# Performance work log

Hardware: AMD Instinct MI355X
Metric: run time of the kernel (lower is better)

Reference implementation:

```python
import math
import jax, jax.numpy as jnp
import numpy as np

B, S, D, H = 2, 2048, 2048, 16
HD = D // H  # 128


def _rope_tables(seq_len, head_dim, theta=10000.0):
    freqs = 1.0 / (theta ** (np.arange(0, head_dim, 2, dtype=np.float32) / head_dim))
    t = np.arange(seq_len, dtype=np.float32)
    ang = np.outer(t, freqs)  # [S, HD/2]
    return jnp.asarray(np.cos(ang)), jnp.asarray(np.sin(ang))


def setup_inputs() -> dict:
    key = jax.random.key(0)
    ks = jax.random.split(key, 5)
    sc = 1.0 / math.sqrt(D)
    x = jax.random.normal(ks[0], (B, S, D), dtype=jnp.float32)
    wq = jax.random.normal(ks[1], (D, D), dtype=jnp.float32) * sc
    wk = jax.random.normal(ks[2], (D, D), dtype=jnp.float32) * sc
    wv = jax.random.normal(ks[3], (D, D), dtype=jnp.float32) * sc
    wo = jax.random.normal(ks[4], (D, D), dtype=jnp.float32) * sc
    freqs_cos, freqs_sin = _rope_tables(S, HD)
    # additive causal mask: 0 on/below diagonal, -inf above
    mask = jnp.where(jnp.tril(jnp.ones((S, S), dtype=bool)), 0.0, -jnp.inf).astype(jnp.float32)
    return {"x": x, "wq": wq, "wk": wk, "wv": wv, "wo": wo,
            "freqs_cos": freqs_cos, "freqs_sin": freqs_sin,
            "mask": mask, "start_pos": 0}


def _apply_rope(t, cos, sin):
    # t: [B, S, H, HD]; pairs (even, odd) rotated as complex numbers (LLaMA style)
    tr = t.reshape(*t.shape[:-1], HD // 2, 2)
    te, to = tr[..., 0], tr[..., 1]
    c = cos[None, :, None, :]
    s = sin[None, :, None, :]
    out_e = te * c - to * s
    out_o = te * s + to * c
    return jnp.stack([out_e, out_o], axis=-1).reshape(t.shape)


def reference(x, wq, wk, wv, wo, freqs_cos, freqs_sin, mask, start_pos):
    bsz, seqlen, _ = x.shape
    xq = (x @ wq.T).reshape(bsz, seqlen, H, HD)
    xk = (x @ wk.T).reshape(bsz, seqlen, H, HD)
    xv = (x @ wv.T).reshape(bsz, seqlen, H, HD)
    xq = _apply_rope(xq, freqs_cos, freqs_sin)
    xk = _apply_rope(xk, freqs_cos, freqs_sin)
    # n_rep == 1 so repeat_kv is identity
    scores = jnp.einsum('bqhd,bkhd->bhqk', xq, xk) / math.sqrt(HD)
    scores = scores + mask  # broadcast [S,S] over [B,H,S,S]
    probs = jax.nn.softmax(scores.astype(jnp.float32), axis=-1).astype(xq.dtype)
    out = jnp.einsum('bhqk,bkhd->bqhd', probs, xv).reshape(bsz, seqlen, -1)
    return out @ wo.T
```

## Files before the change

### kernel.cpp

```cpp
#include <hip/hip_runtime.h>


typedef __bf16 bf16_t;
typedef __bf16 bf16x4 __attribute__((ext_vector_type(4)));
typedef __bf16 bf16x8 __attribute__((ext_vector_type(8)));
typedef float  f32x4  __attribute__((ext_vector_type(4)));

#define DEV __device__ __forceinline__

DEV void async_copy16(const bf16_t* g, bf16_t* lds_uniform_base) {
    __builtin_amdgcn_global_load_lds(
        (const __attribute__((address_space(1))) void*)g,
        (__attribute__((address_space(3))) void*)lds_uniform_base,
        16, 0, 0);
}

__global__ void cast_all(const float* __restrict__ x,  const float* __restrict__ wq,
                         const float* __restrict__ wk, const float* __restrict__ wv,
                         const float* __restrict__ wo,
                         bf16_t* __restrict__ xb, bf16_t* __restrict__ W3,
                         bf16_t* __restrict__ wob)
{
    const int i = blockIdx.x * blockDim.x + threadIdx.x;
    const float4* src;
    bf16x4* dst;
    if (i < 2097152) {
        src = (const float4*)x + i;
        dst = (bf16x4*)xb + i;
    } else {
        const int j   = i - 2097152;
        const int r   = j >> 20;
        const int off = j & 1048575;
        const float* s4 = (r == 0) ? wq : (r == 1) ? wk : (r == 2) ? wv : wo;
        src = (const float4*)s4 + off;
        dst = (r < 3) ? ((bf16x4*)W3 + (long)r * 1048576 + off)
                      : ((bf16x4*)wob + off);
    }
    const float4 v = *src;
    bf16x4 o = { (bf16_t)v.x, (bf16_t)v.y, (bf16_t)v.z, (bf16_t)v.w };
    *dst = o;
}

__global__ __launch_bounds__(256)
void gemm_qkv(const bf16_t* __restrict__ A, const bf16_t* __restrict__ Bm,
              bf16_t* __restrict__ Qo, bf16_t* __restrict__ Ko,
              bf16_t* __restrict__ VTo,
              const float* __restrict__ cosT, const float* __restrict__ sinT)
{
    constexpr int K = 2048;
    __shared__ bf16_t As[128 * 64];
    __shared__ bf16_t Bs[128 * 64];

    const int tid  = threadIdx.x;
    const int w    = tid >> 6;
    const int lane = tid & 63;
    const int l16  = lane & 15;
    const int quad = lane >> 4;
    const int l7   = l16 & 7;
    const int wm   = w >> 1, wn = w & 1;

    const int id   = blockIdx.x;
    const int xcd  = id & 7;
    const int slot = id >> 3;
    const int nl   = slot % 6;
    const int ml   = slot / 6;
    const long n0  = (long)(xcd * 6 + nl) * 128;
    const long m0  = (long)ml * 128;

    f32x4 acc[4][4] = {};

    const bf16_t* Ag[4];
    const bf16_t* Bg[4];
    #pragma unroll
    for (int i = 0; i < 4; ++i) {
        const int c   = i * 256 + tid;
        const int row = c >> 3;
        const int col = ((c & 7) ^ (row & 7)) * 8;
        Ag[i] = A  + (m0 + row) * K + col;
        Bg[i] = Bm + (n0 + row) * K + col;
    }

    for (int k0 = 0; k0 < K; k0 += 64) {
        __syncthreads();
        #pragma unroll
        for (int i = 0; i < 4; ++i) {
            async_copy16(Ag[i] + k0, As + i * 2048 + w * 512);
            async_copy16(Bg[i] + k0, Bs + i * 2048 + w * 512);
        }
        __syncthreads();

        #pragma unroll
        for (int kc = 0; kc < 2; ++kc) {
            bf16x8 af[4], bfr[4];
            #pragma unroll
            for (int t = 0; t < 4; ++t) {
                const int cs = ((kc * 4 + quad) ^ l7) * 8;
                af[t]  = *(const bf16x8*)&As[(wm * 64 + t * 16 + l16) * 64 + cs];
                bfr[t] = *(const bf16x8*)&Bs[(wn * 64 + t * 16 + l16) * 64 + cs];
            }
            #pragma unroll
            for (int mt = 0; mt < 4; ++mt)
                #pragma unroll
                for (int nt = 0; nt < 4; ++nt)
                    acc[mt][nt] = __builtin_amdgcn_mfma_f32_16x16x32_bf16(
                        af[mt], bfr[nt], acc[mt][nt], 0, 0, 0);
        }
    }

    const int region = (int)(n0 >> 11);
    #pragma unroll
    for (int mt = 0; mt < 4; ++mt) {
        #pragma unroll
        for (int nt = 0; nt < 4; ++nt) {
            if (region < 2) {
                bf16_t* dst = (region == 0) ? Qo : Ko;
                #pragma unroll
                for (int r = 0; r < 4; ++r) {
                    const long m = m0 + wm * 64 + mt * 16 + quad * 4 + r;
                    const long n = n0 + wn * 64 + nt * 16 + l16;
                    float v = acc[mt][nt][r];
                    const float partner = __shfl_xor(v, 1);
                    const int d    = (int)n & 127;
                    const int fidx = ((int)m & 2047) * 64 + (d >> 1);
                    const float c = cosT[fidx], s = sinT[fidx];
                    v = ((int)n & 1) ? fmaf(partner, s, v * c)
                                     : (v * c - partner * s);
                    dst[m * 2048 + (n & 2047)] = (bf16_t)v;
                }
            } else {
                const long m  = m0 + wm * 64 + mt * 16 + quad * 4;
                const int  np = (int)(n0 + wn * 64 + nt * 16 + l16) - 4096;
                bf16x4 pk;
                #pragma unroll
                for (int r = 0; r < 4; ++r) pk[r] = (bf16_t)acc[mt][nt][r];
                const int b  = (int)(m >> 11);
                const int s0 = (int)m & 2047;
                const long idx = ((long)(b * 16 + (np >> 7)) * 128 + (np & 127)) * 2048 + s0;
                *(bf16x4*)&VTo[idx] = pk;
            }
        }
    }
}

__global__ __launch_bounds__(256)
void gemm_out(const bf16_t* __restrict__ A, const bf16_t* __restrict__ Bm,
              float* __restrict__ Cp)
{
    constexpr int K = 2048, N = 2048;
    __shared__ bf16_t As[128 * 64];
    __shared__ bf16_t Bs[128 * 64];

    const int tid  = threadIdx.x;
    const int w    = tid >> 6;
    const int lane = tid & 63;
    const int l16  = lane & 15;
    const int quad = lane >> 4;
    const int l7   = l16 & 7;
    const int wm   = w >> 1, wn = w & 1;

    const int id   = blockIdx.x;
    const int xcd  = id & 7;
    const int slot = id >> 3;
    const long n0  = (long)(xcd * 2 + (slot & 1)) * 128;
    const long m0  = (long)(slot >> 1) * 128;

    f32x4 acc[4][4] = {};

    const bf16_t* Ag[4];
    const bf16_t* Bg[4];
    #pragma unroll
    for (int i = 0; i < 4; ++i) {
        const int c   = i * 256 + tid;
        const int row = c >> 3;
        const int col = ((c & 7) ^ (row & 7)) * 8;
        Ag[i] = A  + (m0 + row) * K + col;
        Bg[i] = Bm + (n0 + row) * K + col;
    }

    for (int k0 = 0; k0 < K; k0 += 64) {
        __syncthreads();
        #pragma unroll
        for (int i = 0; i < 4; ++i) {
            async_copy16(Ag[i] + k0, As + i * 2048 + w * 512);
            async_copy16(Bg[i] + k0, Bs + i * 2048 + w * 512);
        }
        __syncthreads();

        #pragma unroll
        for (int kc = 0; kc < 2; ++kc) {
            bf16x8 af[4], bfr[4];
            #pragma unroll
            for (int t = 0; t < 4; ++t) {
                const int cs = ((kc * 4 + quad) ^ l7) * 8;
                af[t]  = *(const bf16x8*)&As[(wm * 64 + t * 16 + l16) * 64 + cs];
                bfr[t] = *(const bf16x8*)&Bs[(wn * 64 + t * 16 + l16) * 64 + cs];
            }
            #pragma unroll
            for (int mt = 0; mt < 4; ++mt)
                #pragma unroll
                for (int nt = 0; nt < 4; ++nt)
                    acc[mt][nt] = __builtin_amdgcn_mfma_f32_16x16x32_bf16(
                        af[mt], bfr[nt], acc[mt][nt], 0, 0, 0);
        }
    }

    #pragma unroll
    for (int mt = 0; mt < 4; ++mt)
        #pragma unroll
        for (int nt = 0; nt < 4; ++nt)
            #pragma unroll
            for (int r = 0; r < 4; ++r) {
                const long m = m0 + wm * 64 + mt * 16 + quad * 4 + r;
                const long n = n0 + wn * 64 + nt * 16 + l16;
                Cp[m * N + n] = acc[mt][nt][r];
            }
}

__global__ __launch_bounds__(256, 2)
void flash_attn(const bf16_t* __restrict__ Q, const bf16_t* __restrict__ Kg,
                const bf16_t* __restrict__ VT, bf16_t* __restrict__ O)
{
    constexpr int S = 2048, D = 2048;
    constexpr int PSTR = 72;
    __shared__ bf16_t Kb[2][64 * 128];
    __shared__ bf16_t Ps[128 * PSTR];

    const int tid  = threadIdx.x;
    const int w    = tid >> 6, lane = tid & 63, l16 = lane & 15, quad = lane >> 4;
    const int l7   = l16 & 7;

    const int id   = blockIdx.x;
    const int half = id >> 8;
    const int rest = id & 255;
    const int xcd  = rest & 7;
    const int s    = rest >> 3;
    const int hh   = s & 3;
    const int qh   = s >> 2;
    const int qt   = half ? (15 - qh) : qh;
    const int bh   = xcd * 4 + hh;
    const int b    = bh >> 4, h = bh & 15;
    const int q0   = qt * 128;

    bf16x8 qf[2][4];
    {
        const bf16_t* qp = Q + (long)(b * S + q0 + w * 32 + l16) * D + h * 128 + quad * 8;
        #pragma unroll
        for (int qi = 0; qi < 2; ++qi)
            #pragma unroll
            for (int kk = 0; kk < 4; ++kk)
                qf[qi][kk] = *(const bf16x8*)(qp + qi * 16 * D + kk * 32);
    }

    int koff[4];
    #pragma unroll
    for (int i = 0; i < 4; ++i) {
        const int c  = i * 256 + tid;
        const int kr = c >> 4, cs = c & 15;
        const int cc = (cs & 8) | ((cs & 7) ^ (kr & 7));
        koff[i] = kr * D + cc * 8;
    }
    const bf16_t* Kst = Kg + (long)b * S * D + h * 128;
    const bf16_t* Vl  = VT + (long)bh * 128 * S + (long)l16 * S + quad * 8;

    f32x4 oacc[2][8] = {};
    float li[2] = { 0.f, 0.f };
    const float SC = 0.08838834764831845f * 1.44269504088896340f;

    const int nkt = 2 * qt + 2;

    #pragma unroll
    for (int i = 0; i < 4; ++i)
        async_copy16(Kst + koff[i], &Kb[0][i * 2048 + w * 512]);
    bf16x8 vf[2][8];
    #pragma unroll
    for (int ks = 0; ks < 2; ++ks)
        #pragma unroll
        for (int nv = 0; nv < 8; ++nv)
            vf[ks][nv] = *(const bf16x8*)(Vl + (long)nv * 16 * S + ks * 32);

    for (int kt = 0; kt < nkt; ++kt) {
        __syncthreads();
        const int knx = (kt + 1 < nkt) ? (kt + 1) : kt;
        #pragma unroll
        for (int i = 0; i < 4; ++i)
            async_copy16(Kst + (long)knx * 64 * D + koff[i],
                         &Kb[(kt + 1) & 1][i * 2048 + w * 512]);

        const bool active = (kt * 64 <= q0 + w * 32 + 31);
        if (active) {
            f32x4 sc[4][2] = {};
            const bf16_t* Kcur = Kb[kt & 1];
            #pragma unroll
            for (int kk = 0; kk < 4; ++kk)
                #pragma unroll
                for (int mt = 0; mt < 4; ++mt) {
                    const int cc = kk * 4 + quad;
                    const bf16x8 kf = *(const bf16x8*)
                        &Kcur[(mt * 16 + l16) * 128 + ((cc & 8) | ((cc & 7) ^ l7)) * 8];
                    sc[mt][0] = __builtin_amdgcn_mfma_f32_16x16x32_bf16(
                        kf, qf[0][kk], sc[mt][0], 0, 0, 0);
                    sc[mt][1] = __builtin_amdgcn_mfma_f32_16x16x32_bf16(
                        kf, qf[1][kk], sc[mt][1], 0, 0, 0);
                }

            #pragma unroll
            for (int qi = 0; qi < 2; ++qi) {
                const int qg = q0 + w * 32 + qi * 16 + l16;
                float rs = 0.f;
                #pragma unroll
                for (int mt = 0; mt < 4; ++mt) {
                    bf16x4 pk;
                    #pragma unroll
                    for (int r = 0; r < 4; ++r) {
                        const int kg = kt * 64 + mt * 16 + quad * 4 + r;
                        const float p = (kg > qg) ? 0.f
                                      : exp2f(sc[mt][qi][r] * SC - 24.0f);
                        rs += p;
                        pk[r] = (bf16_t)p;
                    }
                    *(bf16x4*)&Ps[(w * 32 + qi * 16 + l16) * PSTR + mt * 16 + quad * 4] = pk;
                }
                li[qi] += rs;
            }

            #pragma unroll
            for (int ks = 0; ks < 2; ++ks) {
                const bf16x8 pf0 = *(const bf16x8*)
                    &Ps[(w * 32 + l16) * PSTR + ks * 32 + quad * 8];
                const bf16x8 pf1 = *(const bf16x8*)
                    &Ps[(w * 32 + 16 + l16) * PSTR + ks * 32 + quad * 8];
                #pragma unroll
                for (int nv = 0; nv < 8; ++nv) {
                    const bf16x8 vcur = vf[ks][nv];
                    vf[ks][nv] = *(const bf16x8*)
                        (Vl + (long)nv * 16 * S + ks * 32 + (long)knx * 64);
                    oacc[0][nv] = __builtin_amdgcn_mfma_f32_16x16x32_bf16(
                        pf0, vcur, oacc[0][nv], 0, 0, 0);
                    oacc[1][nv] = __builtin_amdgcn_mfma_f32_16x16x32_bf16(
                        pf1, vcur, oacc[1][nv], 0, 0, 0);
                }
            }
        }
    }

    #pragma unroll
    for (int qi = 0; qi < 2; ++qi) {
        li[qi] += __shfl_xor(li[qi], 16);
        li[qi] += __shfl_xor(li[qi], 32);
        const float inv = 1.0f / li[qi];
        #pragma unroll
        for (int r = 0; r < 4; ++r) {
            const float invr = __shfl(inv, quad * 4 + r);
            const long  row  = (long)(b * S + q0 + w * 32 + qi * 16 + quad * 4 + r);
            #pragma unroll
            for (int nv = 0; nv < 8; ++nv)
                O[row * D + h * 128 + nv * 16 + l16] = (bf16_t)(oacc[qi][nv][r] * invr);
        }
    }
}

extern "C" void kernel_launch(void* const* d_in, const int* in_sizes, int n_in,
                              void* d_out, int out_size, void* d_ws, size_t ws_size,
                              hipStream_t stream) {
    const float* x  = (const float*)d_in[0];
    const float* wq = (const float*)d_in[1];
    const float* wk = (const float*)d_in[2];
    const float* wv = (const float*)d_in[3];
    const float* wo = (const float*)d_in[4];
    const float* fc = (const float*)d_in[5];
    const float* fs = (const float*)d_in[6];

    char* ws = (char*)d_ws;
    bf16_t* xb  = (bf16_t*)(ws + 0);
    bf16_t* W3  = (bf16_t*)(ws + (16l << 20));
    bf16_t* wob = (bf16_t*)(ws + (40l << 20));
    bf16_t* Qb  = (bf16_t*)(ws + (48l << 20));
    bf16_t* Kb  = (bf16_t*)(ws + (64l << 20));
    bf16_t* VTb = (bf16_t*)(ws + (80l << 20));
    bf16_t* Ob  = xb;

    cast_all<<<24576, 256, 0, stream>>>(x, wq, wk, wv, wo, xb, W3, wob);

    gemm_qkv<<<1536, 256, 0, stream>>>(xb, W3, Qb, Kb, VTb, fc, fs);

    flash_attn<<<512, 256, 0, stream>>>(Qb, Kb, VTb, Ob);

    gemm_out<<<512, 256, 0, stream>>>(Ob, wob, (float*)d_out);
}
```

Baseline: 431.4 us.

## Pair causal query tiles per block in attention and shrink out-GEMM K tile

Flash attention now uses 64-row query tiles, one 16-row slice per wave. Each block handles a long and a short tile (qt and 31-p), so causal work is balanced across blocks and the per-wave inactive-tile check disappears. K and V prefetch carries over between the two jobs, and the P tile moves to a 64x64 XOR-swizzled LDS layout. Separately, the output GEMM halves its K step to 32 and drops its swizzle, which doubles the number of barriers per K and may cause LDS bank conflicts.

Result: slower. 465.6 us (+7.9%).

```diff
diff --git a/kernel.cpp b/kernel.cpp
--- a/kernel.cpp
+++ b/kernel.cpp
@@ -147,15 +147,14 @@
               float* __restrict__ Cp)
 {
     constexpr int K = 2048, N = 2048;
-    __shared__ bf16_t As[128 * 64];
-    __shared__ bf16_t Bs[128 * 64];
+    __shared__ bf16_t As[128 * 32];
+    __shared__ bf16_t Bs[128 * 32];
 
     const int tid  = threadIdx.x;
     const int w    = tid >> 6;
     const int lane = tid & 63;
     const int l16  = lane & 15;
     const int quad = lane >> 4;
-    const int l7   = l16 & 7;
     const int wm   = w >> 1, wn = w & 1;
 
     const int id   = blockIdx.x;
@@ -166,42 +165,31 @@
 
     f32x4 acc[4][4] = {};
 
-    const bf16_t* Ag[4];
-    const bf16_t* Bg[4];
-    #pragma unroll
-    for (int i = 0; i < 4; ++i) {
-        const int c   = i * 256 + tid;
-        const int row = c >> 3;
-        const int col = ((c & 7) ^ (row & 7)) * 8;
-        Ag[i] = A  + (m0 + row) * K + col;
-        Bg[i] = Bm + (n0 + row) * K + col;
-    }
-
-    for (int k0 = 0; k0 < K; k0 += 64) {
+    const int srow = tid >> 2;
+    const int soff = (tid & 3) * 8;
+    const bf16_t* Ag = A  + (m0 + srow) * K + soff;
+    const bf16_t* Bg = Bm + (n0 + srow) * K + soff;
+
+    for (int k0 = 0; k0 < K; k0 += 32) {
         __syncthreads();
-        #pragma unroll
-        for (int i = 0; i < 4; ++i) {
-            async_copy16(Ag[i] + k0, As + i * 2048 + w * 512);
-            async_copy16(Bg[i] + k0, Bs + i * 2048 + w * 512);
-        }
+        async_copy16(Ag + k0,          As + w * 512);
+        async_copy16(Ag + 64 * K + k0, As + 2048 + w * 512);
+        async_copy16(Bg + k0,          Bs + w * 512);
+        async_copy16(Bg + 64 * K + k0, Bs + 2048 + w * 512);
         __syncthreads();
 
-        #pragma unroll
-        for (int kc = 0; kc < 2; ++kc) {
-            bf16x8 af[4], bfr[4];
-            #pragma unroll
-            for (int t = 0; t < 4; ++t) {
-                const int cs = ((kc * 4 + quad) ^ l7) * 8;
-                af[t]  = *(const bf16x8*)&As[(wm * 64 + t * 16 + l16) * 64 + cs];
-                bfr[t] = *(const bf16x8*)&Bs[(wn * 64 + t * 16 + l16) * 64 + cs];
-            }
-            #pragma unroll
-            for (int mt = 0; mt < 4; ++mt)
-                #pragma unroll
-                for (int nt = 0; nt < 4; ++nt)
-                    acc[mt][nt] = __builtin_amdgcn_mfma_f32_16x16x32_bf16(
-                        af[mt], bfr[nt], acc[mt][nt], 0, 0, 0);
-        }
+        bf16x8 af[4], bfr[4];
+        #pragma unroll
+        for (int t = 0; t < 4; ++t) {
+            af[t]  = *(const bf16x8*)&As[(wm * 64 + t * 16 + l16) * 32 + quad * 8];
+            bfr[t] = *(const bf16x8*)&Bs[(wn * 64 + t * 16 + l16) * 32 + quad * 8];
+        }
+        #pragma unroll
+        for (int mt = 0; mt < 4; ++mt)
+            #pragma unroll
+            for (int nt = 0; nt < 4; ++nt)
+                acc[mt][nt] = __builtin_amdgcn_mfma_f32_16x16x32_bf16(
+                    af[mt], bfr[nt], acc[mt][nt], 0, 0, 0);
     }
 
     #pragma unroll
@@ -221,35 +209,17 @@
                 const bf16_t* __restrict__ VT, bf16_t* __restrict__ O)
 {
     constexpr int S = 2048, D = 2048;
-    constexpr int PSTR = 72;
     __shared__ bf16_t Kb[2][64 * 128];
-    __shared__ bf16_t Ps[128 * PSTR];
+    __shared__ bf16_t Ps[64 * 64];
 
     const int tid  = threadIdx.x;
     const int w    = tid >> 6, lane = tid & 63, l16 = lane & 15, quad = lane >> 4;
     const int l7   = l16 & 7;
 
     const int id   = blockIdx.x;
-    const int half = id >> 8;
-    const int rest = id & 255;
-    const int xcd  = rest & 7;
-    const int s    = rest >> 3;
-    const int hh   = s & 3;
-    const int qh   = s >> 2;
-    const int qt   = half ? (15 - qh) : qh;
-    const int bh   = xcd * 4 + hh;
+    const int bh   = id & 31;
+    const int p    = id >> 5;
     const int b    = bh >> 4, h = bh & 15;
-    const int q0   = qt * 128;
-
-    bf16x8 qf[2][4];
-    {
-        const bf16_t* qp = Q + (long)(b * S + q0 + w * 32 + l16) * D + h * 128 + quad * 8;
-        #pragma unroll
-        for (int qi = 0; qi < 2; ++qi)
-            #pragma unroll
-            for (int kk = 0; kk < 4; ++kk)
-                qf[qi][kk] = *(const bf16x8*)(qp + qi * 16 * D + kk * 32);
-    }
 
     int koff[4];
     #pragma unroll
@@ -262,11 +232,7 @@
     const bf16_t* Kst = Kg + (long)b * S * D + h * 128;
     const bf16_t* Vl  = VT + (long)bh * 128 * S + (long)l16 * S + quad * 8;
 
-    f32x4 oacc[2][8] = {};
-    float li[2] = { 0.f, 0.f };
     const float SC = 0.08838834764831845f * 1.44269504088896340f;
-
-    const int nkt = 2 * qt + 2;
 
     #pragma unroll
     for (int i = 0; i < 4; ++i)
@@ -278,18 +244,33 @@
         for (int nv = 0; nv < 8; ++nv)
             vf[ks][nv] = *(const bf16x8*)(Vl + (long)nv * 16 * S + ks * 32);
 
-    for (int kt = 0; kt < nkt; ++kt) {
-        __syncthreads();
-        const int knx = (kt + 1 < nkt) ? (kt + 1) : kt;
-        #pragma unroll
-        for (int i = 0; i < 4; ++i)
-            async_copy16(Kst + (long)knx * 64 * D + koff[i],
-                         &Kb[(kt + 1) & 1][i * 2048 + w * 512]);
-
-        const bool active = (kt * 64 <= q0 + w * 32 + 31);
-        if (active) {
-            f32x4 sc[4][2] = {};
-            const bf16_t* Kcur = Kb[kt & 1];
+    int g = 0;
+    for (int job = 0; job < 2; ++job) {
+        const int qt = job ? p : (31 - p);
+        const int q0 = qt * 64;
+
+        bf16x8 qf[4];
+        {
+            const bf16_t* qp = Q + (long)(b * S + q0 + w * 16 + l16) * D
+                                 + h * 128 + quad * 8;
+            #pragma unroll
+            for (int kk = 0; kk < 4; ++kk)
+                qf[kk] = *(const bf16x8*)(qp + kk * 32);
+        }
+
+        f32x4 oacc[8] = {};
+        float li = 0.f;
+
+        for (int kt = 0; kt <= qt; ++kt, ++g) {
+            __syncthreads();
+            const int nk = (kt < qt) ? kt + 1 : (job == 0 ? 0 : kt);
+            #pragma unroll
+            for (int i = 0; i < 4; ++i)
+                async_copy16(Kst + (long)nk * 64 * D + koff[i],
+                             &Kb[(g + 1) & 1][i * 2048 + w * 512]);
+
+            f32x4 sc[4] = {};
+            const bf16_t* Kcur = Kb[g & 1];
             #pragma unroll
             for (int kk = 0; kk < 4; ++kk)
                 #pragma unroll
@@ -297,64 +278,54 @@
                     const int cc = kk * 4 + quad;
                     const bf16x8 kf = *(const bf16x8*)
                         &Kcur[(mt * 16 + l16) * 128 + ((cc & 8) | ((cc & 7) ^ l7)) * 8];
-                    sc[mt][0] = __builtin_amdgcn_mfma_f32_16x16x32_bf16(
-                        kf, qf[0][kk], sc[mt][0], 0, 0, 0);
-                    sc[mt][1] = __builtin_amdgcn_mfma_f32_16x16x32_bf16(
-                        kf, qf[1][kk], sc[mt][1], 0, 0, 0);
+                    sc[mt] = __builtin_amdgcn_mfma_f32_16x16x32_bf16(
+                        kf, qf[kk], sc[mt], 0, 0, 0);
                 }
 
-            #pragma unroll
-            for (int qi = 0; qi < 2; ++qi) {
-                const int qg = q0 + w * 32 + qi * 16 + l16;
-                float rs = 0.f;
-                #pragma unroll
-                for (int mt = 0; mt < 4; ++mt) {
-                    bf16x4 pk;
-                    #pragma unroll
-                    for (int r = 0; r < 4; ++r) {
-                        const int kg = kt * 64 + mt * 16 + quad * 4 + r;
-                        const float p = (kg > qg) ? 0.f
-                                      : exp2f(sc[mt][qi][r] * SC - 24.0f);
-                        rs += p;
-                        pk[r] = (bf16_t)p;
-                    }
-                    *(bf16x4*)&Ps[(w * 32 + qi * 16 + l16) * PSTR + mt * 16 + quad * 4] = pk;
+            const bool diag = (kt == qt);
+            const int qloc  = w * 16 + l16;
+            float rs = 0.f;
+            #pragma unroll
+            for (int mt = 0; mt < 4; ++mt) {
+                bf16x4 pk;
+                #pragma unroll
+                for (int r = 0; r < 4; ++r) {
+                    const int kloc = mt * 16 + quad * 4 + r;
+                    const float pv = (diag && kloc > qloc) ? 0.f
+                                   : exp2f(sc[mt][r] * SC - 24.0f);
+                    rs += pv;
+                    pk[r] = (bf16_t)pv;
                 }
-                li[qi] += rs;
-            }
+                const int slot = (mt * 2 + (quad >> 1)) ^ l7;
+                *(bf16x4*)&Ps[(w * 16 + l16) * 64 + slot * 8 + (quad & 1) * 4] = pk;
+            }
+            li += rs;
 
             #pragma unroll
             for (int ks = 0; ks < 2; ++ks) {
-                const bf16x8 pf0 = *(const bf16x8*)
-                    &Ps[(w * 32 + l16) * PSTR + ks * 32 + quad * 8];
-                const bf16x8 pf1 = *(const bf16x8*)
-                    &Ps[(w * 32 + 16 + l16) * PSTR + ks * 32 + quad * 8];
+                const bf16x8 pf = *(const bf16x8*)
+                    &Ps[(w * 16 + l16) * 64 + ((ks * 4 + quad) ^ l7) * 8];
                 #pragma unroll
                 for (int nv = 0; nv < 8; ++nv) {
                     const bf16x8 vcur = vf[ks][nv];
                     vf[ks][nv] = *(const bf16x8*)
-                        (Vl + (long)nv * 16 * S + ks * 32 + (long)knx * 64);
-                    oacc[0][nv] = __builtin_amdgcn_mfma_f32_16x16x32_bf16(
-                        pf0, vcur, oacc[0][nv], 0, 0, 0);
-                    oacc[1][nv] = __builtin_amdgcn_mfma_f32_16x16x32_bf16(
-                        pf1, vcur, oacc[1][nv], 0, 0, 0);
+                        (Vl + (long)nv * 16 * S + ks * 32 + (long)nk * 64);
+                    oacc[nv] = __builtin_amdgcn_mfma_f32_16x16x32_bf16(
+                        pf, vcur, oacc[nv], 0, 0, 0);
                 }
             }
         }
-    }
-
-    #pragma unroll
-    for (int qi = 0; qi < 2; ++qi) {
-        li[qi] += __shfl_xor(li[qi], 16);
-        li[qi] += __shfl_xor(li[qi], 32);
-        const float inv = 1.0f / li[qi];
+
+        li += __shfl_xor(li, 16);
+        li += __shfl_xor(li, 32);
+        const float inv = 1.0f / li;
         #pragma unroll
         for (int r = 0; r < 4; ++r) {
             const float invr = __shfl(inv, quad * 4 + r);
-            const long  row  = (long)(b * S + q0 + w * 32 + qi * 16 + quad * 4 + r);
+            const long  row  = (long)(b * S + q0 + w * 16 + quad * 4 + r);
             #pragma unroll
             for (int nv = 0; nv < 8; ++nv)
-                O[row * D + h * 128 + nv * 16 + l16] = (bf16_t)(oacc[qi][nv][r] * invr);
+                O[row * D + h * 128 + nv * 16 + l16] = (bf16_t)(oacc[nv][r] * invr);
         }
     }
 }
```
